# Performance work log

Measured on AMD Instinct MI355X. Metric: run time of the kernel, lower is better.

The kernel has to match this reference:

```python
import jax, jax.numpy as jnp
import numpy as np

# ---- static config (matches init_kwargs) ----
B, S, E = 1, 2048, 2048
H, G, D = 32, 8, 64            # query heads, kv groups, head_dim
GS = H // G                    # group size = 4
SW = 128                       # sliding window
LAYER_IDX = 0                  # even -> sliding-window mask active
ROPE_BASE = 10000.0
ORIG_CTX = 4096.0              # yarn_original_context_length
YARN_SCALE = 2.0               # yarn_scaling_factor
BETA_FAST, BETA_SLOW = 32.0, 1.0


def _rope_sincos(position_ids):
    # YaRN-adjusted RoPE angles, computed directly at position_ids.
    freqs = 1.0 / ROPE_BASE ** (jnp.arange(0, D, 2, dtype=jnp.float32) / D)  # [D/2]
    wave_len = 2.0 * jnp.pi / freqs
    low = ORIG_CTX / BETA_FAST
    high = ORIG_CTX / BETA_SLOW
    t = jnp.clip((wave_len - low) / (high - low), 0.0, 1.0)
    eff = freqs * (1.0 - t) + (freqs / YARN_SCALE) * t
    conc = 0.1 * jnp.log(jnp.float32(YARN_SCALE)) + 1.0
    ang = position_ids[..., None].astype(jnp.float32) * eff * conc           # [B,S,D/2]
    ang = jnp.concatenate([ang, ang], axis=-1)                               # [B,S,D]
    # add head axis for broadcast over [B,H,S,D]
    return jnp.sin(ang)[:, None], jnp.cos(ang)[:, None]


def _apply_rope(x, sin, cos):
    x1, x2 = x[..., : D // 2], x[..., D // 2 :]
    rotated = jnp.concatenate([-x2, x1], axis=-1)
    return x * cos + rotated * sin


def setup_inputs() -> dict:
    key = jax.random.key(0)
    ks = jax.random.split(key, 6)
    x = jax.random.normal(ks[0], (B, S, E), dtype=jnp.float32)
    position_ids = jnp.broadcast_to(jnp.arange(S, dtype=jnp.int32), (B, S))
    # additive causal mask: -inf above the diagonal
    i = jnp.arange(S)[:, None]
    j = jnp.arange(S)[None, :]
    attn_mask = jnp.where(j > i, -jnp.inf, 0.0).astype(jnp.float32)[None, None]  # [1,1,S,S]
    sc = 0.02
    Wqkv = jax.random.normal(ks[1], ((H + 2 * G) * D, E), dtype=jnp.float32) * sc
    bqkv = jax.random.normal(ks[2], ((H + 2 * G) * D,), dtype=jnp.float32) * sc
    Wout = jax.random.normal(ks[3], (E, H * D), dtype=jnp.float32) * sc
    bout = jax.random.normal(ks[4], (E,), dtype=jnp.float32) * sc
    sinks = jax.random.normal(ks[5], (1, H, 1, 1), dtype=jnp.float32)
    return {"x": x, "position_ids": position_ids, "attn_mask": attn_mask,
            "Wqkv": Wqkv, "bqkv": bqkv, "Wout": Wout, "bout": bout, "sinks": sinks}


def reference(x, position_ids, attn_mask, Wqkv, bqkv, Wout, bout, sinks):
    b, s, _ = x.shape
    qkv = (x @ Wqkv.T + bqkv).reshape(b, s, H + 2 * G, D)
    Q = qkv[:, :, :H].transpose(0, 2, 1, 3)              # [B,H,S,D]
    K = qkv[:, :, H : H + G].transpose(0, 2, 1, 3)       # [B,G,S,D]
    V = qkv[:, :, H + G :].transpose(0, 2, 1, 3)         # [B,G,S,D]

    sin, cos = _rope_sincos(position_ids)
    Q = _apply_rope(Q, sin, cos)
    K = _apply_rope(K, sin, cos)

    # GQA: group query heads, no K/V duplication
    Qg = Q.reshape(b, G, GS, s, D)
    scores = jnp.einsum("bgmqd,bgkd->bgmqk", Qg, K) / (D ** 0.5)  # [B,G,GS,S,S]
    scores = scores.reshape(b, H, s, s) + attn_mask

    # sliding-window mask (layer_idx even, kv_len > sliding_window)
    if LAYER_IDX % 2 == 0 and s > SW:
        i = jnp.arange(s)[:, None]
        j = jnp.arange(s)[None, :]
        scores = jnp.where(j <= i - SW, -jnp.inf, scores)

    # learned sink logit prepended before softmax, then dropped
    sink = jnp.broadcast_to(sinks, (b, H, s, 1))
    attn = jax.nn.softmax(jnp.concatenate([sink, scores], axis=-1), axis=-1)[..., 1:]

    ctx = jnp.einsum("bgmqk,bgkd->bgmqd", attn.reshape(b, G, GS, s, s), V)
    ctx = ctx.reshape(b, H, s, D).transpose(0, 2, 1, 3).reshape(b, s, H * D)
    return ctx @ Wout.T + bout
```

## Files before the change

kernel.cpp:

```cpp
#include <hip/hip_runtime.h>
#include <cstdint>

#define S_LEN 2048
#define EMB   2048
#define NHEAD 32
#define NKV   8
#define HDIM  64
#define NQKV  3072

typedef __attribute__((ext_vector_type(8))) short bf16x8;
typedef __attribute__((ext_vector_type(4))) float f32x4;

#define GPTR const __attribute__((address_space(1))) void*
#define LPTR __attribute__((address_space(3))) void*

__device__ __forceinline__ unsigned short f2bf(float f){
  union { float f; unsigned int u; } v; v.f = f;
  unsigned int r = v.u + 0x7FFFu + ((v.u >> 16) & 1u);
  return (unsigned short)(r >> 16);
}
__device__ __forceinline__ float bf2f(unsigned short u){
  union { unsigned int u; float f; } v; v.u = ((unsigned int)u) << 16;
  return v.f;
}
__device__ __forceinline__ float yarn_eff(float ifr){
  const float freq = __expf(-ifr * (9.210340371976184f / 32.0f));
  const float wl = 6.283185307179586f / freq;
  float t = fminf(fmaxf((wl - 128.0f) * (1.0f / 3968.0f), 0.f), 1.f);
  return freq * (1.0f - 0.5f * t) * 1.0693147180559945f;
}

__global__ __launch_bounds__(256) void cvt3_kernel(const float* __restrict__ a, unsigned short* __restrict__ da, int na,
                                                   const float* __restrict__ b, unsigned short* __restrict__ db, int nb,
                                                   const float* __restrict__ c, unsigned short* __restrict__ dc, int nc){
  int i = blockIdx.x * 256 + threadIdx.x;
  const float* s; unsigned short* d;
  if (i < na){ s = a; d = da; }
  else if (i < na + nb){ s = b; d = db; i -= na; }
  else if (i < na + nb + nc){ s = c; d = dc; i -= na + nb; }
  else return;
  const float4 v = ((const float4*)s)[i];
  ushort4 o;
  o.x = f2bf(v.x); o.y = f2bf(v.y); o.z = f2bf(v.z); o.w = f2bf(v.w);
  ((ushort4*)d)[i] = o;
}

template<int OUT_BF16, int ROPE>
__global__ __launch_bounds__(256) void gemm_bt(const unsigned short* __restrict__ A,
                                               const unsigned short* __restrict__ B,
                                               const float* __restrict__ bias,
                                               void* __restrict__ Cout,
                                               const int* __restrict__ pos,
                                               int M, int N, int K){
  __shared__ unsigned short As[3*128*32];
  __shared__ unsigned short Bs[3*128*32];
  const int tid  = threadIdx.x;
  const int lane = tid & 63;
  const int wid  = tid >> 6;
  const int m0 = blockIdx.y * 128;
  const int n0 = blockIdx.x * 128;
  const int wm = (wid >> 1) * 64;
  const int wn = (wid & 1) * 64;
  const int fm = lane & 15;
  const int q8 = (lane >> 4) * 8;
  const int quad = lane >> 4;

  f32x4 acc[4][4];
#pragma unroll
  for (int i = 0; i < 4; ++i)
#pragma unroll
    for (int j = 0; j < 4; ++j) acc[i][j] = {0.f, 0.f, 0.f, 0.f};

  const int srow = lane >> 2;
  const int scol = (lane & 3) * 8;
  const unsigned short* Ag = A + (size_t)(m0 + wid*32 + srow) * K + scol;
  const unsigned short* Bg = B + (size_t)(n0 + wid*32 + srow) * K + scol;
  unsigned short* AsW = &As[(wid*32)*32];
  unsigned short* BsW = &Bs[(wid*32)*32];

  auto stage = [&](int k0, int buf){
    unsigned short* dA = AsW + buf*(128*32);
    unsigned short* dB = BsW + buf*(128*32);
    __builtin_amdgcn_global_load_lds((GPTR)(Ag + k0), (LPTR)dA, 16, 0, 0);
    __builtin_amdgcn_global_load_lds((GPTR)(Ag + k0 + (size_t)16*K), (LPTR)(dA + 16*32), 16, 0, 0);
    __builtin_amdgcn_global_load_lds((GPTR)(Bg + k0), (LPTR)dB, 16, 0, 0);
    __builtin_amdgcn_global_load_lds((GPTR)(Bg + k0 + (size_t)16*K), (LPTR)(dB + 16*32), 16, 0, 0);
  };

  stage(0, 0);
  stage(32, 1);

  const int KITER = K >> 5;
  int bcur = 0;
  for (int it = 0; it < KITER; ++it){
    if (it + 1 < KITER) asm volatile("s_waitcnt vmcnt(4)" ::: "memory");
    else                asm volatile("s_waitcnt vmcnt(0)" ::: "memory");
    asm volatile("s_barrier" ::: "memory");
    if (it + 2 < KITER){
      int bnext = bcur + 2; if (bnext >= 3) bnext -= 3;
      stage((it + 2) * 32, bnext);
    }
    const unsigned short* Ab = As + bcur*(128*32);
    const unsigned short* Bb = Bs + bcur*(128*32);
    bf16x8 af[4], bfr[4];
#pragma unroll
    for (int i = 0; i < 4; ++i) af[i]  = *(const bf16x8*)&Ab[(wm + i*16 + fm)*32 + q8];
#pragma unroll
    for (int j = 0; j < 4; ++j) bfr[j] = *(const bf16x8*)&Bb[(wn + j*16 + fm)*32 + q8];
#pragma unroll
    for (int i = 0; i < 4; ++i)
#pragma unroll
      for (int j = 0; j < 4; ++j)
        acc[i][j] = __builtin_amdgcn_mfma_f32_16x16x32_bf16(af[i], bfr[j], acc[i][j], 0, 0, 0);
    bcur = (bcur == 2) ? 0 : bcur + 1;
  }

  float bv[4];
#pragma unroll
  for (int j = 0; j < 4; ++j) bv[j] = bias[n0 + wn + j*16 + fm];

  const bool dorope = ROPE && (n0 + wn) < 2560;
  if (dorope){
    const float eff0 = yarn_eff((float)fm);
    const float eff1 = yarn_eff((float)(fm + 16));
#pragma unroll
    for (int i = 0; i < 4; ++i){
#pragma unroll
      for (int r = 0; r < 4; ++r){
        const int row = m0 + wm + i*16 + quad*4 + r;
        const float pp = (float)pos[row];
        float s0, c0, s1, c1;
        __sincosf(pp * eff0, &s0, &c0);
        __sincosf(pp * eff1, &s1, &c1);
        const float v0 = acc[i][0][r] + bv[0];
        const float v1 = acc[i][1][r] + bv[1];
        const float v2 = acc[i][2][r] + bv[2];
        const float v3 = acc[i][3][r] + bv[3];
        const float o0 = v0*c0 - v2*s0;
        const float o1 = v1*c1 - v3*s1;
        const float o2 = v2*c0 + v0*s0;
        const float o3 = v3*c1 + v1*s1;
        const size_t base = (size_t)row*N + n0 + wn + fm;
        if (OUT_BF16){
          unsigned short* C16 = (unsigned short*)Cout;
          C16[base +  0] = f2bf(o0); C16[base + 16] = f2bf(o1);
          C16[base + 32] = f2bf(o2); C16[base + 48] = f2bf(o3);
        } else {
          float* C32 = (float*)Cout;
          C32[base +  0] = o0; C32[base + 16] = o1;
          C32[base + 32] = o2; C32[base + 48] = o3;
        }
      }
    }
  } else {
#pragma unroll
    for (int i = 0; i < 4; ++i){
#pragma unroll
      for (int r = 0; r < 4; ++r){
        const int row = m0 + wm + i*16 + quad*4 + r;
        const size_t base = (size_t)row*N + n0 + wn + fm;
#pragma unroll
        for (int j = 0; j < 4; ++j){
          const float v = acc[i][j][r] + bv[j];
          if (OUT_BF16) ((unsigned short*)Cout)[base + j*16] = f2bf(v);
          else          ((float*)Cout)[base + j*16] = v;
        }
      }
    }
  }
}

__global__ __launch_bounds__(256) void attn_kernel(const unsigned short* __restrict__ qkv,
                                                   const float* __restrict__ sinks,
                                                   unsigned short* __restrict__ ctxb){
  const int h  = blockIdx.y;
  const int q0 = blockIdx.x * 64;
  const int g  = h >> 2;
  const int tid  = threadIdx.x;
  const int lane = tid & 63;
  const int wid  = tid >> 6;
  const int fm   = lane & 15;
  const int quad = lane >> 4;

  __shared__ unsigned short Ks[2*64*40];
  __shared__ unsigned short Vt[2*64*34];
  __shared__ unsigned short Pl[4*2*16*40];

  const int qrow = q0 + wid*16 + fm;
  bf16x8 aq[2];
#pragma unroll
  for (int ks = 0; ks < 2; ++ks)
    aq[ks] = *(const bf16x8*)(qkv + (size_t)qrow*NQKV + h*HDIM + ks*32 + quad*8);

  f32x4 o[4];
#pragma unroll
  for (int nt = 0; nt < 4; ++nt) o[nt] = {0.f, 0.f, 0.f, 0.f};
  float m_[4], l_[4];
#pragma unroll
  for (int r = 0; r < 4; ++r){ m_[r] = -30000.f; l_[r] = 0.f; }

  const int qbase = q0 + wid*16 + quad*4;
  int cs0 = q0 - 128; if (cs0 < 0) cs0 = 0;
  unsigned short* plw = &Pl[wid*1280];

  for (int cs = cs0; cs <= q0; cs += 64){
    __syncthreads();
#pragma unroll
    for (int it = 0; it < 2; ++it){
      const int e = (tid + it*256) * 8;
      const int key = e >> 6, d0 = e & 63;
      const unsigned short* kp = qkv + (size_t)(cs + key)*NQKV + EMB + g*HDIM + d0;
      *(bf16x8*)&Ks[(d0>>5)*2560 + key*40 + (d0 & 31)] = *(const bf16x8*)kp;
      const bf16x8 vv = *(const bf16x8*)(kp + NKV*HDIM);
      const unsigned short* vs = (const unsigned short*)&vv;
      unsigned short* vt = &Vt[(key>>5)*2176 + (key & 31)];
#pragma unroll
      for (int j = 0; j < 8; ++j) vt[(d0 + j)*34] = vs[j];
    }
    __syncthreads();

    f32x4 sa[4];
#pragma unroll
    for (int nt = 0; nt < 4; ++nt){
      sa[nt] = {0.f, 0.f, 0.f, 0.f};
#pragma unroll
      for (int ks = 0; ks < 2; ++ks){
        const bf16x8 bk = *(const bf16x8*)&Ks[ks*2560 + (nt*16 + fm)*40 + quad*8];
        sa[nt] = __builtin_amdgcn_mfma_f32_16x16x32_bf16(aq[ks], bk, sa[nt], 0, 0, 0);
      }
    }

#pragma unroll
    for (int nt = 0; nt < 4; ++nt){
      const int key = cs + nt*16 + fm;
#pragma unroll
      for (int r = 0; r < 4; ++r){
        const float s = sa[nt][r] * 0.125f;
        const bool ok = (unsigned)(qbase + r - key) < 128u;
        sa[nt][r] = ok ? s : -1e30f;
      }
    }

#pragma unroll
    for (int r = 0; r < 4; ++r){
      float t = fmaxf(fmaxf(sa[0][r], sa[1][r]), fmaxf(sa[2][r], sa[3][r]));
#pragma unroll
      for (int off = 1; off < 16; off <<= 1) t = fmaxf(t, __shfl_xor(t, off, 64));
      const float nm = fmaxf(m_[r], t);
      const float al = __expf(m_[r] - nm);
#pragma unroll
      for (int nt = 0; nt < 4; ++nt) sa[nt][r] = __expf(sa[nt][r] - nm);
      float ts = (sa[0][r] + sa[1][r]) + (sa[2][r] + sa[3][r]);
#pragma unroll
      for (int off = 1; off < 16; off <<= 1) ts += __shfl_xor(ts, off, 64);
      l_[r] = l_[r]*al + ts;
      m_[r] = nm;
#pragma unroll
      for (int nt = 0; nt < 4; ++nt) o[nt][r] *= al;
    }

#pragma unroll
    for (int nt = 0; nt < 4; ++nt)
#pragma unroll
      for (int r = 0; r < 4; ++r)
        plw[(nt>>1)*640 + (quad*4 + r)*40 + (nt&1)*16 + fm] = f2bf(sa[nt][r]);
    __asm__ volatile("s_waitcnt lgkmcnt(0)" ::: "memory");

    bf16x8 pa[2];
#pragma unroll
    for (int ks = 0; ks < 2; ++ks)
      pa[ks] = *(const bf16x8*)&plw[ks*640 + fm*40 + quad*8];
    const unsigned int* vb = (const unsigned int*)Vt;
#pragma unroll
    for (int nt = 0; nt < 4; ++nt){
#pragma unroll
      for (int ks = 0; ks < 2; ++ks){
        const int ui = ks*1088 + (nt*16 + fm)*17 + quad*4;
        union { unsigned int u[4]; bf16x8 v; } bb;
        bb.u[0] = vb[ui+0]; bb.u[1] = vb[ui+1]; bb.u[2] = vb[ui+2]; bb.u[3] = vb[ui+3];
        o[nt] = __builtin_amdgcn_mfma_f32_16x16x32_bf16(pa[ks], bb.v, o[nt], 0, 0, 0);
      }
    }
  }

  const float snk = sinks[h];
#pragma unroll
  for (int r = 0; r < 4; ++r){
    const float nm = fmaxf(m_[r], snk);
    const float e  = __expf(m_[r] - nm);
    const float denom = l_[r]*e + __expf(snk - nm);
    const float sc = e / denom;
    const size_t row = (size_t)(qbase + r)*EMB + h*HDIM;
#pragma unroll
    for (int nt = 0; nt < 4; ++nt)
      ctxb[row + nt*16 + fm] = f2bf(o[nt][r] * sc);
  }
}

extern "C" void kernel_launch(void* const* d_in, const int* in_sizes, int n_in,
                              void* d_out, int out_size, void* d_ws, size_t ws_size,
                              hipStream_t stream){
  const float* x     = (const float*)d_in[0];
  const int*   pos   = (const int*)  d_in[1];
  const float* Wqkv  = (const float*)d_in[3];
  const float* bqkv  = (const float*)d_in[4];
  const float* Wout  = (const float*)d_in[5];
  const float* bout  = (const float*)d_in[6];
  const float* sinks = (const float*)d_in[7];

  char* ws = (char*)d_ws;
  unsigned short* xb   = (unsigned short*)(ws);
  unsigned short* wqb  = (unsigned short*)(ws + 8388608);
  unsigned short* wob  = (unsigned short*)(ws + 20971520);
  unsigned short* qkv  = (unsigned short*)(ws + 29360128);
  unsigned short* ctxb = (unsigned short*)(ws + 41943040);

  cvt3_kernel<<<dim3(14336), dim3(256), 0, stream>>>(x, xb, 1048576,
                                                     Wqkv, wqb, 1572864,
                                                     Wout, wob, 1048576);

  gemm_bt<1,1><<<dim3(24, 16), dim3(256), 0, stream>>>(xb, wqb, bqkv, (void*)qkv, pos, 2048, 3072, 2048);
  attn_kernel<<<dim3(32, 32), dim3(256), 0, stream>>>(qkv, sinks, ctxb);
  gemm_bt<0,0><<<dim3(16, 16), dim3(256), 0, stream>>>(ctxb, wob, bout, d_out, nullptr, 2048, 2048, 2048);
}
```

Baseline: 225.3 us.

## Restructure GEMM pipeline to 64-wide K epochs and use 64-row tiles for output projection

The GEMM main loop now processes two 32-wide K sub-tiles per iteration (64-wide epochs) with a four-slot, double-buffered LDS ring. Loads for epoch e+2 are issued after a second barrier at the end of each epoch, which halves the number of barrier/wait points per K. A template tile-height parameter lets the output projection use 64-row tiles, doubling its grid to 512 blocks so the GPU's many CUs are better occupied. In exchange, each block uses more LDS, there is an extra barrier per epoch, and the smaller tiles reuse the B operand less.

New measurement: 198.9 us. 11.7% less time.

```diff
diff --git a/kernel.cpp b/kernel.cpp
--- a/kernel.cpp
+++ b/kernel.cpp
@@ -45,74 +45,89 @@
   ((ushort4*)d)[i] = o;
 }
 
-template<int OUT_BF16, int ROPE>
+template<int OUT_BF16, int ROPE, int TM>
 __global__ __launch_bounds__(256) void gemm_bt(const unsigned short* __restrict__ A,
                                                const unsigned short* __restrict__ B,
                                                const float* __restrict__ bias,
                                                void* __restrict__ Cout,
                                                const int* __restrict__ pos,
                                                int M, int N, int K){
-  __shared__ unsigned short As[3*128*32];
-  __shared__ unsigned short Bs[3*128*32];
+  constexpr int MI = TM / 32;
+  constexpr int AI = TM / 64;
+  constexpr int VI = 2 * (AI + 2);
+  __shared__ unsigned short As[4*TM*32];
+  __shared__ unsigned short Bs[4*128*32];
   const int tid  = threadIdx.x;
   const int lane = tid & 63;
   const int wid  = tid >> 6;
-  const int m0 = blockIdx.y * 128;
+  const int m0 = blockIdx.y * TM;
   const int n0 = blockIdx.x * 128;
-  const int wm = (wid >> 1) * 64;
+  const int wm = (wid >> 1) * (TM/2);
   const int wn = (wid & 1) * 64;
   const int fm = lane & 15;
   const int q8 = (lane >> 4) * 8;
   const int quad = lane >> 4;
 
-  f32x4 acc[4][4];
-#pragma unroll
-  for (int i = 0; i < 4; ++i)
+  f32x4 acc[MI][4];
+#pragma unroll
+  for (int i = 0; i < MI; ++i)
 #pragma unroll
     for (int j = 0; j < 4; ++j) acc[i][j] = {0.f, 0.f, 0.f, 0.f};
 
   const int srow = lane >> 2;
   const int scol = (lane & 3) * 8;
-  const unsigned short* Ag = A + (size_t)(m0 + wid*32 + srow) * K + scol;
+  const unsigned short* Ag = A + (size_t)(m0 + wid*(TM/4) + srow) * K + scol;
   const unsigned short* Bg = B + (size_t)(n0 + wid*32 + srow) * K + scol;
-  unsigned short* AsW = &As[(wid*32)*32];
+  unsigned short* AsW = &As[(wid*(TM/4))*32];
   unsigned short* BsW = &Bs[(wid*32)*32];
 
-  auto stage = [&](int k0, int buf){
-    unsigned short* dA = AsW + buf*(128*32);
-    unsigned short* dB = BsW + buf*(128*32);
-    __builtin_amdgcn_global_load_lds((GPTR)(Ag + k0), (LPTR)dA, 16, 0, 0);
-    __builtin_amdgcn_global_load_lds((GPTR)(Ag + k0 + (size_t)16*K), (LPTR)(dA + 16*32), 16, 0, 0);
+  auto stage_sub = [&](int k0, int slot){
+    unsigned short* dA = AsW + slot*(TM*32);
+    unsigned short* dB = BsW + slot*(128*32);
+#pragma unroll
+    for (int t = 0; t < AI; ++t)
+      __builtin_amdgcn_global_load_lds((GPTR)(Ag + k0 + (size_t)(t*16)*K), (LPTR)(dA + t*16*32), 16, 0, 0);
     __builtin_amdgcn_global_load_lds((GPTR)(Bg + k0), (LPTR)dB, 16, 0, 0);
     __builtin_amdgcn_global_load_lds((GPTR)(Bg + k0 + (size_t)16*K), (LPTR)(dB + 16*32), 16, 0, 0);
   };
 
-  stage(0, 0);
-  stage(32, 1);
-
-  const int KITER = K >> 5;
-  int bcur = 0;
-  for (int it = 0; it < KITER; ++it){
-    if (it + 1 < KITER) asm volatile("s_waitcnt vmcnt(4)" ::: "memory");
-    else                asm volatile("s_waitcnt vmcnt(0)" ::: "memory");
+  stage_sub(0, 0);  stage_sub(32, 1);
+  stage_sub(64, 2); stage_sub(96, 3);
+
+  const int KEP = K >> 6;
+  for (int e = 0; e < KEP; ++e){
+    const int buf = e & 1;
+    if (e + 1 < KEP){
+      if constexpr (TM == 128) asm volatile("s_waitcnt vmcnt(8)" ::: "memory");
+      else                     asm volatile("s_waitcnt vmcnt(6)" ::: "memory");
+    } else {
+      asm volatile("s_waitcnt vmcnt(0)" ::: "memory");
+    }
     asm volatile("s_barrier" ::: "memory");
-    if (it + 2 < KITER){
-      int bnext = bcur + 2; if (bnext >= 3) bnext -= 3;
-      stage((it + 2) * 32, bnext);
-    }
-    const unsigned short* Ab = As + bcur*(128*32);
-    const unsigned short* Bb = Bs + bcur*(128*32);
-    bf16x8 af[4], bfr[4];
-#pragma unroll
-    for (int i = 0; i < 4; ++i) af[i]  = *(const bf16x8*)&Ab[(wm + i*16 + fm)*32 + q8];
-#pragma unroll
-    for (int j = 0; j < 4; ++j) bfr[j] = *(const bf16x8*)&Bb[(wn + j*16 + fm)*32 + q8];
-#pragma unroll
-    for (int i = 0; i < 4; ++i)
-#pragma unroll
-      for (int j = 0; j < 4; ++j)
-        acc[i][j] = __builtin_amdgcn_mfma_f32_16x16x32_bf16(af[i], bfr[j], acc[i][j], 0, 0, 0);
-    bcur = (bcur == 2) ? 0 : bcur + 1;
+
+    bf16x8 af[2][MI], bfr[2][4];
+#pragma unroll
+    for (int s = 0; s < 2; ++s){
+      const unsigned short* Ab = As + (buf*2+s)*(TM*32);
+      const unsigned short* Bb = Bs + (buf*2+s)*(128*32);
+#pragma unroll
+      for (int i = 0; i < MI; ++i) af[s][i]  = *(const bf16x8*)&Ab[(wm + i*16 + fm)*32 + q8];
+#pragma unroll
+      for (int j = 0; j < 4; ++j)  bfr[s][j] = *(const bf16x8*)&Bb[(wn + j*16 + fm)*32 + q8];
+    }
+#pragma unroll
+    for (int s = 0; s < 2; ++s)
+#pragma unroll
+      for (int i = 0; i < MI; ++i)
+#pragma unroll
+        for (int j = 0; j < 4; ++j)
+          acc[i][j] = __builtin_amdgcn_mfma_f32_16x16x32_bf16(af[s][i], bfr[s][j], acc[i][j], 0, 0, 0);
+
+    asm volatile("s_barrier" ::: "memory");
+    if (e + 2 < KEP){
+      stage_sub((e+2)*64,      buf*2);
+      stage_sub((e+2)*64 + 32, buf*2 + 1);
+    }
   }
 
   float bv[4];
@@ -124,7 +139,7 @@
     const float eff0 = yarn_eff((float)fm);
     const float eff1 = yarn_eff((float)(fm + 16));
 #pragma unroll
-    for (int i = 0; i < 4; ++i){
+    for (int i = 0; i < MI; ++i){
 #pragma unroll
       for (int r = 0; r < 4; ++r){
         const int row = m0 + wm + i*16 + quad*4 + r;
@@ -154,7 +169,7 @@
     }
   } else {
 #pragma unroll
-    for (int i = 0; i < 4; ++i){
+    for (int i = 0; i < MI; ++i){
 #pragma unroll
       for (int r = 0; r < 4; ++r){
         const int row = m0 + wm + i*16 + quad*4 + r;
@@ -319,7 +334,7 @@
                                                      Wqkv, wqb, 1572864,
                                                      Wout, wob, 1048576);
 
-  gemm_bt<1,1><<<dim3(24, 16), dim3(256), 0, stream>>>(xb, wqb, bqkv, (void*)qkv, pos, 2048, 3072, 2048);
+  gemm_bt<1,1,128><<<dim3(24, 16), dim3(256), 0, stream>>>(xb, wqb, bqkv, (void*)qkv, pos, 2048, 3072, 2048);
   attn_kernel<<<dim3(32, 32), dim3(256), 0, stream>>>(qkv, sinks, ctxb);
-  gemm_bt<0,0><<<dim3(16, 16), dim3(256), 0, stream>>>(ctxb, wob, bout, d_out, nullptr, 2048, 2048, 2048);
-}
+  gemm_bt<0,0,64><<<dim3(16, 32), dim3(256), 0, stream>>>(ctxb, wob, bout, d_out, nullptr, 2048, 2048, 2048);
+}
```
